# Kernel optimization log

Measured on AMD Instinct MI355X. Metric: run time of the kernel, lower is better.

The kernel has to match this reference:

```python
import jax, jax.numpy as jnp
import numpy as np

B, S, D, H, KH, DH, L, V, MULT = 1, 2048, 2048, 16, 2, 128, 4, 10000, 4
INNER = D * MULT
EPS = 1e-5


def layernorm(x, g, b):
    m = jnp.mean(x, axis=-1, keepdims=True)
    v = jnp.var(x, axis=-1, keepdims=True)
    return (x - m) * jax.lax.rsqrt(v + EPS) * g + b


def setup_inputs() -> dict:
    key = jax.random.key(0)
    ks = jax.random.split(key, 24)
    s = lambda *shape: 0.02
    inp = {
        'text': jax.random.randint(ks[0], (B, S), 0, V),
        'embed_w': jax.random.normal(ks[1], (V, D), jnp.float32) * 0.02,
        # model-level LayerNorm (applied after embed and after every block)
        'model_norm_g': jnp.ones((D,), jnp.float32),
        'model_norm_b': jnp.zeros((D,), jnp.float32),
        # per-block params, stacked on leading L axis
        'blk_norm_g': jnp.ones((L, D), jnp.float32),
        'blk_norm_b': jnp.zeros((L, D), jnp.float32),
        'attn_norm_g': jnp.ones((L, D), jnp.float32),  # RingAttention prenorm
        'attn_norm_b': jnp.zeros((L, D), jnp.float32),
        'wq': jax.random.normal(ks[2], (L, D, H * DH), jnp.float32) * 0.02,
        'wk': jax.random.normal(ks[3], (L, D, KH * DH), jnp.float32) * 0.02,
        'wv': jax.random.normal(ks[4], (L, D, KH * DH), jnp.float32) * 0.02,
        'wo': jax.random.normal(ks[5], (L, H * DH, D), jnp.float32) * 0.02,
        'qn_g': jnp.ones((L, DH), jnp.float32),  # qk_norm LayerNorm scales
        'kn_g': jnp.ones((L, DH), jnp.float32),
        'w1': jax.random.normal(ks[6], (L, D, INNER), jnp.float32) * 0.02,
        'b1': jnp.zeros((L, INNER), jnp.float32),
        'w2': jax.random.normal(ks[7], (L, INNER, D), jnp.float32) * 0.02,
        'b2': jnp.zeros((L, D), jnp.float32),
        # output head: LayerNorm + Linear(D, V)
        'head_norm_g': jnp.ones((D,), jnp.float32),
        'head_norm_b': jnp.zeros((D,), jnp.float32),
        'head_w': jax.random.normal(ks[8], (D, V), jnp.float32) * 0.02,
        'head_b': jnp.zeros((V,), jnp.float32),
    }
    return inp


def _attention(xn, wq, wk, wv, wo, qn_g, kn_g):
    # xn: [B,S,D] (already prenormed)
    q = (xn @ wq).reshape(B, S, H, DH)
    k = (xn @ wk).reshape(B, S, KH, DH)
    v = (xn @ wv).reshape(B, S, KH, DH)
    # qk-norm: LayerNorm over head dim with learnable scale
    q = layernorm(q, qn_g, 0.0)
    k = layernorm(k, kn_g, 0.0)
    # GQA: expand kv heads to query heads
    rep = H // KH
    k = jnp.repeat(k, rep, axis=2)  # [B,S,H,DH]
    v = jnp.repeat(v, rep, axis=2)
    scale = DH ** -0.5
    scores = jnp.einsum('bqhd,bkhd->bhqk', q, k) * scale  # [B,H,S,S]
    causal = jnp.tril(jnp.ones((S, S), bool))
    scores = jnp.where(causal, scores, jnp.finfo(scores.dtype).min)
    p = jax.nn.softmax(scores, axis=-1)
    out = jnp.einsum('bhqk,bkhd->bqhd', p, v).reshape(B, S, H * DH)
    return out @ wo


def reference(text, embed_w, model_norm_g, model_norm_b, blk_norm_g, blk_norm_b,
              attn_norm_g, attn_norm_b, wq, wk, wv, wo, qn_g, kn_g,
              w1, b1, w2, b2, head_norm_g, head_norm_b, head_w, head_b):
    x = embed_w[text]                                # [B,S,D]
    x = layernorm(x, model_norm_g, model_norm_b)
    for i in range(L):
        h = layernorm(x, blk_norm_g[i], blk_norm_b[i])       # block norm
        hn = layernorm(h, attn_norm_g[i], attn_norm_b[i])    # attn prenorm
        h = _attention(hn, wq[i], wk[i], wv[i], wo[i], qn_g[i], kn_g[i]) + h
        ff = jax.nn.gelu(h @ w1[i] + b1[i]) @ w2[i] + b2[i]
        x = ff + h
        x = layernorm(x, model_norm_g, model_norm_b)
    x = layernorm(x, head_norm_g, head_norm_b)
    return x @ head_w + head_b                       # [B,S,V] logits
```

## Files before the change

### kernel.cpp

```cpp
#include <hip/hip_runtime.h>
#include <math.h>

#define S_LEN 2048
#define DMODEL 2048
#define NHEAD 16
#define KVHEAD 2
#define DHEAD 128
#define NLAYER 4
#define VOCAB 10000
#define INNER_DIM 8192
#define LN_EPS 1e-5f
#define VOCAB_PAD 10240
#define QKVN 2560

typedef __attribute__((ext_vector_type(4))) float f32x4;
typedef __attribute__((ext_vector_type(2))) float f32x2;
typedef __attribute__((ext_vector_type(8))) short s16x8;
typedef __attribute__((ext_vector_type(4))) short s16x4;

__device__ __forceinline__ short f2bf(float f) {
  union { float f; unsigned u; } v; v.f = f;
  unsigned r = v.u + 0x7FFFu + ((v.u >> 16) & 1u);
  return (short)(r >> 16);
}

__device__ __forceinline__ float gelu_tanh(float x) {
  float z = 0.7978845608028654f * (x + 0.044715f * x * x * x);
  float t = __expf(-2.0f * fabsf(z));
  float th = (1.0f - t) / (1.0f + t);
  th = copysignf(th, z);
  return 0.5f * x * (1.0f + th);
}

__device__ __forceinline__ void glds16(const void* g, void* l) {
  __builtin_amdgcn_global_load_lds(
      (const __attribute__((address_space(1))) unsigned int*)g,
      (__attribute__((address_space(3))) unsigned int*)l, 16, 0, 0);
}

__global__ __launch_bounds__(256)
void wtrans_all(const float* __restrict__ wq, const float* __restrict__ wk,
                const float* __restrict__ wv, const float* __restrict__ wo,
                const float* __restrict__ w1, const float* __restrict__ w2,
                short* __restrict__ wqkvT, short* __restrict__ woT,
                short* __restrict__ w1T, short* __restrict__ w2T) {
  __shared__ float ld[64][65];
  int b = blockIdx.x;
  const float* W; short* WT; int gx, K;
  if (b < 1024)      { W = wq; WT = wqkvT; gx = 32; K = 2048; }
  else if (b < 1152) { b -= 1024; W = wk; WT = wqkvT + (size_t)2048 * 2048; gx = 4; K = 2048; }
  else if (b < 1280) { b -= 1152; W = wv; WT = wqkvT + (size_t)2304 * 2048; gx = 4; K = 2048; }
  else if (b < 2304) { b -= 1280; W = wo; WT = woT; gx = 32; K = 2048; }
  else if (b < 6400) { b -= 2304; W = w1; WT = w1T; gx = 128; K = 2048; }
  else               { b -= 6400; W = w2; WT = w2T; gx = 32; K = 8192; }
  const int N = gx * 64;
  const int n0 = (b % gx) * 64, k0 = (b / gx) * 64;
  const int tid = threadIdx.x;
  const int rbase = tid >> 4;
  const int c4 = (tid & 15) * 4;
#pragma unroll
  for (int q = 0; q < 4; ++q) {
    int kk = rbase + q * 16;
    f32x4 v = *(const f32x4*)(W + (size_t)(k0 + kk) * N + n0 + c4);
    ld[kk][c4 + 0] = v[0]; ld[kk][c4 + 1] = v[1];
    ld[kk][c4 + 2] = v[2]; ld[kk][c4 + 3] = v[3];
  }
  __syncthreads();
#pragma unroll
  for (int s = 0; s < 2; ++s) {
    int lin = tid + s * 256;
    int nn = lin >> 3;
    int ks = lin & 7;
    s16x8 o;
#pragma unroll
    for (int j = 0; j < 8; ++j) o[j] = f2bf(ld[ks * 8 + j][nn]);
    *(s16x8*)&WT[(size_t)(n0 + nn) * K + k0 + ks * 8] = o;
  }
}

__global__ __launch_bounds__(256)
void wtrans64(const float* __restrict__ W, short* __restrict__ WT,
              int K, int N, int NP) {
  __shared__ float ld[64][65];
  const int n0 = blockIdx.x * 64, k0 = blockIdx.y * 64;
  const int tid = threadIdx.x;
  const int rbase = tid >> 4;
  const int c4 = (tid & 15) * 4;
#pragma unroll
  for (int q = 0; q < 4; ++q) {
    int kk = rbase + q * 16;
    const float* wp = W + (size_t)(k0 + kk) * N + n0 + c4;
    float v0, v1, v2, v3;
    if (n0 + c4 + 3 < N) {
      f32x4 v = *(const f32x4*)wp;
      v0 = v[0]; v1 = v[1]; v2 = v[2]; v3 = v[3];
    } else {
      v0 = (n0 + c4 + 0 < N) ? wp[0] : 0.f;
      v1 = (n0 + c4 + 1 < N) ? wp[1] : 0.f;
      v2 = (n0 + c4 + 2 < N) ? wp[2] : 0.f;
      v3 = (n0 + c4 + 3 < N) ? wp[3] : 0.f;
    }
    ld[kk][c4 + 0] = v0; ld[kk][c4 + 1] = v1;
    ld[kk][c4 + 2] = v2; ld[kk][c4 + 3] = v3;
  }
  __syncthreads();
#pragma unroll
  for (int s = 0; s < 2; ++s) {
    int lin = tid + s * 256;
    int nn = lin >> 3;
    int ks = lin & 7;
    int n = n0 + nn;
    if (n < NP) {
      s16x8 o;
#pragma unroll
      for (int j = 0; j < 8; ++j)
        o[j] = (n < N) ? f2bf(ld[ks * 8 + j][nn]) : (short)0;
      *(s16x8*)&WT[(size_t)n * K + k0 + ks * 8] = o;
    }
  }
}

__device__ __forceinline__ void ln3_core(
    float (&v)[8], int tid, int wave,
    const float* __restrict__ mg, const float* __restrict__ mb,
    const float* __restrict__ bg, const float* __restrict__ bb,
    const float* __restrict__ ag, const float* __restrict__ ab,
    float* __restrict__ hbrow, short* __restrict__ hnrow,
    float rs[3][4], float rs2[3][4]) {
#pragma unroll
  for (int rnd = 0; rnd < 3; ++rnd) {
    float s = 0.f, s2 = 0.f;
#pragma unroll
    for (int i = 0; i < 8; ++i) { s += v[i]; s2 += v[i] * v[i]; }
#pragma unroll
    for (int off = 1; off < 64; off <<= 1) {
      s += __shfl_xor(s, off); s2 += __shfl_xor(s2, off);
    }
    if ((tid & 63) == 0) { rs[rnd][wave] = s; rs2[rnd][wave] = s2; }
    __syncthreads();
    s = rs[rnd][0] + rs[rnd][1] + rs[rnd][2] + rs[rnd][3];
    s2 = rs2[rnd][0] + rs2[rnd][1] + rs2[rnd][2] + rs2[rnd][3];
    const float mean = s * (1.f / DMODEL);
    const float var = s2 * (1.f / DMODEL) - mean * mean;
    const float rstd = rsqrtf(var + LN_EPS);
    const float* gg = (rnd == 0) ? mg : (rnd == 1) ? bg : ag;
    const float* bbv = (rnd == 0) ? mb : (rnd == 1) ? bb : ab;
#pragma unroll
    for (int i = 0; i < 8; ++i) {
      int idx = tid + i * 256;
      v[i] = (v[i] - mean) * rstd * gg[idx] + bbv[idx];
    }
    if (rnd == 1) {
#pragma unroll
      for (int i = 0; i < 8; ++i) hbrow[tid + i * 256] = v[i];
    }
  }
#pragma unroll
  for (int i = 0; i < 8; ++i) hnrow[tid + i * 256] = f2bf(v[i]);
}

__global__ __launch_bounds__(256)
void ln_triple(const float* __restrict__ in,
               const float* __restrict__ mg, const float* __restrict__ mb,
               const float* __restrict__ bg, const float* __restrict__ bb,
               const float* __restrict__ ag, const float* __restrict__ ab,
               float* __restrict__ hb, short* __restrict__ hn16) {
  const int row = blockIdx.x;
  const int tid = threadIdx.x;
  const int wave = tid >> 6;
  __shared__ float rs[3][4], rs2[3][4];
  float v[8];
  const float* x = in + (size_t)row * DMODEL;
#pragma unroll
  for (int i = 0; i < 8; ++i) v[i] = x[tid + i * 256];
  ln3_core(v, tid, wave, mg, mb, bg, bb, ag, ab,
           hb + (size_t)row * DMODEL, hn16 + (size_t)row * DMODEL, rs, rs2);
}

__global__ __launch_bounds__(256)
void embed_ln3(const int* __restrict__ text, const float* __restrict__ ew,
               const float* __restrict__ mg, const float* __restrict__ mb,
               const float* __restrict__ bg, const float* __restrict__ bb,
               const float* __restrict__ ag, const float* __restrict__ ab,
               float* __restrict__ hb, short* __restrict__ hn16) {
  const int row = blockIdx.x;
  const int tid = threadIdx.x;
  const int wave = tid >> 6;
  __shared__ float rs[3][4], rs2[3][4];
  float v[8];
  const float* x = ew + (size_t)text[row] * DMODEL;
#pragma unroll
  for (int i = 0; i < 8; ++i) v[i] = x[tid + i * 256];
  ln3_core(v, tid, wave, mg, mb, bg, bb, ag, ab,
           hb + (size_t)row * DMODEL, hn16 + (size_t)row * DMODEL, rs, rs2);
}

__global__ __launch_bounds__(256)
void ln_dual(const float* __restrict__ in,
             const float* __restrict__ mg, const float* __restrict__ mb,
             const float* __restrict__ hg, const float* __restrict__ hbv,
             short* __restrict__ out16) {
  const int row = blockIdx.x;
  const int tid = threadIdx.x;
  const int wave = tid >> 6;
  __shared__ float rs[2][4], rs2[2][4];
  float v[8];
  const float* x = in + (size_t)row * DMODEL;
#pragma unroll
  for (int i = 0; i < 8; ++i) v[i] = x[tid + i * 256];
#pragma unroll
  for (int rnd = 0; rnd < 2; ++rnd) {
    float s = 0.f, s2 = 0.f;
#pragma unroll
    for (int i = 0; i < 8; ++i) { s += v[i]; s2 += v[i] * v[i]; }
#pragma unroll
    for (int off = 1; off < 64; off <<= 1) {
      s += __shfl_xor(s, off); s2 += __shfl_xor(s2, off);
    }
    if ((tid & 63) == 0) { rs[rnd][wave] = s; rs2[rnd][wave] = s2; }
    __syncthreads();
    s = rs[rnd][0] + rs[rnd][1] + rs[rnd][2] + rs[rnd][3];
    s2 = rs2[rnd][0] + rs2[rnd][1] + rs2[rnd][2] + rs2[rnd][3];
    const float mean = s * (1.f / DMODEL);
    const float var = s2 * (1.f / DMODEL) - mean * mean;
    const float rstd = rsqrtf(var + LN_EPS);
    const float* gg = (rnd == 0) ? mg : hg;
    const float* bbv = (rnd == 0) ? mb : hbv;
#pragma unroll
    for (int i = 0; i < 8; ++i) {
      int idx = tid + i * 256;
      v[i] = (v[i] - mean) * rstd * gg[idx] + bbv[idx];
    }
  }
  short* o = out16 + (size_t)row * DMODEL;
#pragma unroll
  for (int i = 0; i < 8; ++i) o[tid + i * 256] = f2bf(v[i]);
}

__global__ __launch_bounds__(256)
void normqk_vtrans(const float* __restrict__ qkvf,
                   const float* __restrict__ qg, const float* __restrict__ kg,
                   short* __restrict__ qb16, short* __restrict__ kb16,
                   short* __restrict__ vt) {
  __shared__ float ld[64][65];
  if (blockIdx.x < 9216) {
    const int rowjob = blockIdx.x * 4 + (threadIdx.x >> 6);
    const int lane = threadIdx.x & 63;
    const int s = rowjob / 18, sub = rowjob - s * 18;
    const float* p; short* o; const float* g;
    if (sub < 16) {
      p = qkvf + (size_t)s * QKVN + sub * DHEAD;
      o = qb16 + ((size_t)s * 16 + sub) * DHEAD;
      g = qg;
    } else {
      p = qkvf + (size_t)s * QKVN + 2048 + (sub - 16) * DHEAD;
      o = kb16 + ((size_t)s * 2 + (sub - 16)) * DHEAD;
      g = kg;
    }
    f32x2 t = *(const f32x2*)(p + lane * 2);
    float sm = t[0] + t[1];
    float s2 = t[0] * t[0] + t[1] * t[1];
#pragma unroll
    for (int off = 1; off < 64; off <<= 1) {
      sm += __shfl_xor(sm, off); s2 += __shfl_xor(s2, off);
    }
    const float mean = sm * (1.f / DHEAD);
    const float var = s2 * (1.f / DHEAD) - mean * mean;
    const float rstd = rsqrtf(var + LN_EPS);
    o[lane * 2] = f2bf((t[0] - mean) * rstd * g[lane * 2]);
    o[lane * 2 + 1] = f2bf((t[1] - mean) * rstd * g[lane * 2 + 1]);
  } else {
    const int b = blockIdx.x - 9216;
    const int n0 = (b & 3) * 64, k0 = (b >> 2) * 64;
    const int tid = threadIdx.x;
    const int rbase = tid >> 4;
    const int c4 = (tid & 15) * 4;
#pragma unroll
    for (int q = 0; q < 4; ++q) {
      int kk = rbase + q * 16;
      f32x4 v = *(const f32x4*)(qkvf + (size_t)(k0 + kk) * QKVN + 2304 + n0 + c4);
      ld[kk][c4 + 0] = v[0]; ld[kk][c4 + 1] = v[1];
      ld[kk][c4 + 2] = v[2]; ld[kk][c4 + 3] = v[3];
    }
    __syncthreads();
#pragma unroll
    for (int s = 0; s < 2; ++s) {
      int lin = tid + s * 256;
      int nn = lin >> 3;
      int ks = lin & 7;
      s16x8 o;
#pragma unroll
      for (int j = 0; j < 8; ++j) o[j] = f2bf(ld[ks * 8 + j][nn]);
      *(s16x8*)&vt[(size_t)(n0 + nn) * S_LEN + k0 + ks * 8] = o;
    }
  }
}

template<int BM, int BN, int BK, int WM, int WN, int ACT, bool BIAS, bool RES,
         bool WF, bool WB>
__global__ __launch_bounds__(WM * WN * 64)
void gemm_db(const short* __restrict__ A, const short* __restrict__ BT,
             const float* __restrict__ bias, const float* __restrict__ res,
             float* __restrict__ Cf, short* __restrict__ Cb,
             int M, int N, int K) {
  constexpr int THREADS = WM * WN * 64;
  constexpr int MR = BM / WM / 16;
  constexpr int NR = BN / WN / 16;
  constexpr int KH = BK / 32;
  constexpr int SLOTS = BK / 8;
  constexpr int SMASK = SLOTS - 1;
  constexpr int RSH = (SLOTS == 8) ? 0 : 1;
  constexpr int CSH = (SLOTS == 8) ? 3 : 2;
  constexpr int NI = (BM * BK) / (THREADS * 8);
  __shared__ short As[2][BM * BK];
  __shared__ short Bs[2][BN * BK];
  const int tid = threadIdx.x;
  const int wave = tid >> 6, lane = tid & 63;
  const int g = lane >> 4, r = lane & 15;
  const int wm = wave / WN, wn = wave % WN;

  const int GY = gridDim.y;
  int lin = blockIdx.x + blockIdx.y * gridDim.x;
  int nwg = gridDim.x * GY;
  int sw = ((nwg & 7) == 0) ? ((lin & 7) * (nwg >> 3) + (lin >> 3)) : lin;
  const int bm = (sw % GY) * BM;
  const int bn = (sw / GY) * BN;

  const short* gsrc[2 * NI];
  short* ldst[2][2 * NI];
#pragma unroll
  for (int i = 0; i < NI; ++i) {
    int c = i * THREADS + tid;
    int row = c >> CSH;
    int slot = c & SMASK;
    int col = ((slot ^ ((row >> RSH) & SMASK)) << 3);
    gsrc[i] = A + (size_t)(bm + row) * K + col;
    gsrc[NI + i] = BT + (size_t)(bn + row) * K + col;
    int base = (i * THREADS + (wave << 6)) << 3;
    ldst[0][i] = &As[0][base]; ldst[0][NI + i] = &Bs[0][base];
    ldst[1][i] = &As[1][base]; ldst[1][NI + i] = &Bs[1][base];
  }

  f32x4 acc[MR][NR] = {};
  const int NT = K / BK;

#pragma unroll
  for (int i = 0; i < 2 * NI; ++i) glds16(gsrc[i], ldst[0][i]);
  asm volatile("s_waitcnt vmcnt(0)" ::: "memory");
  __syncthreads();

  for (int t = 0; t < NT; ++t) {
    const int cur = t & 1;
    const short* as = As[cur];
    const short* bs = Bs[cur];
    s16x8 bfr[NR][KH], af[MR / 2][KH];
#pragma unroll
    for (int n = 0; n < NR; ++n) {
      int rr = wn * (NR * 16) + n * 16 + r;
#pragma unroll
      for (int kk = 0; kk < KH; ++kk) {
        int lg = kk * 4 + g;
        bfr[n][kk] = *(const s16x8*)&bs[rr * BK + ((lg ^ ((rr >> RSH) & SMASK)) << 3)];
      }
    }
#pragma unroll
    for (int mm = 0; mm < MR / 2; ++mm) {
      int rr = wm * (MR * 16) + mm * 16 + r;
#pragma unroll
      for (int kk = 0; kk < KH; ++kk) {
        int lg = kk * 4 + g;
        af[mm][kk] = *(const s16x8*)&as[rr * BK + ((lg ^ ((rr >> RSH) & SMASK)) << 3)];
      }
    }
    if (t + 1 < NT) {
#pragma unroll
      for (int i = 0; i < 2 * NI; ++i) glds16(gsrc[i] + (t + 1) * BK, ldst[cur ^ 1][i]);
    }
    asm volatile("s_waitcnt lgkmcnt(0)" ::: "memory");
    __builtin_amdgcn_sched_barrier(0);
    __builtin_amdgcn_s_setprio(1);
#pragma unroll
    for (int mm = 0; mm < MR / 2; ++mm)
#pragma unroll
      for (int n = 0; n < NR; ++n)
#pragma unroll
        for (int kk = 0; kk < KH; ++kk)
          acc[mm][n] = __builtin_amdgcn_mfma_f32_16x16x32_bf16(af[mm][kk], bfr[n][kk], acc[mm][n], 0, 0, 0);
    __builtin_amdgcn_s_setprio(0);
    __builtin_amdgcn_s_barrier();
#pragma unroll
    for (int mm = 0; mm < MR / 2; ++mm) {
      int rr = wm * (MR * 16) + (MR / 2 + mm) * 16 + r;
#pragma unroll
      for (int kk = 0; kk < KH; ++kk) {
        int lg = kk * 4 + g;
        af[mm][kk] = *(const s16x8*)&as[rr * BK + ((lg ^ ((rr >> RSH) & SMASK)) << 3)];
      }
    }
    asm volatile("s_waitcnt lgkmcnt(0)" ::: "memory");
    __builtin_amdgcn_sched_barrier(0);
    __builtin_amdgcn_s_setprio(1);
#pragma unroll
    for (int mm = 0; mm < MR / 2; ++mm)
#pragma unroll
      for (int n = 0; n < NR; ++n)
#pragma unroll
        for (int kk = 0; kk < KH; ++kk)
          acc[MR / 2 + mm][n] = __builtin_amdgcn_mfma_f32_16x16x32_bf16(af[mm][kk], bfr[n][kk], acc[MR / 2 + mm][n], 0, 0, 0);
    __builtin_amdgcn_s_setprio(0);
    __syncthreads();
  }

#pragma unroll
  for (int m = 0; m < MR; ++m) {
    int row = bm + wm * (MR * 16) + m * 16 + g * 4;
#pragma unroll
    for (int n = 0; n < NR; ++n) {
      int col = bn + wn * (NR * 16) + n * 16 + r;
      if (col < N) {
#pragma unroll
        for (int j = 0; j < 4; ++j) {
          float v = acc[m][n][j];
          if (BIAS) v += bias[col];
          if (ACT) v = gelu_tanh(v);
          if (RES) v += res[(size_t)(row + j) * N + col];
          if (WF) Cf[(size_t)(row + j) * N + col] = v;
          if (WB) Cb[(size_t)(row + j) * N + col] = f2bf(v);
        }
      }
    }
  }
}

template<int ACT, bool BIAS, bool WF, bool WB>
__global__ __launch_bounds__(512, 2)
void gemm_8ph(const short* __restrict__ A, const short* __restrict__ BT,
              const float* __restrict__ bias,
              float* __restrict__ Cf, short* __restrict__ Cb,
              int M, int N, int K) {
  __shared__ short As[2][2][128 * 64];
  __shared__ short Bs[2][2][128 * 64];
  const int tid = threadIdx.x;
  const int wave = tid >> 6, lane = tid & 63;
  const int g = lane >> 4, r = lane & 15;
  const int wm = wave >> 2, wn = wave & 3;

  const int GY = gridDim.y;
  int lin = blockIdx.x + blockIdx.y * gridDim.x;
  int nwg = gridDim.x * GY;
  int sw = (lin & 7) * (nwg >> 3) + (lin >> 3);
  const int bm = (sw % GY) * 256;
  const int bn = (sw / GY) * 256;

  int rl[2], csw[2], ldo[2];
#pragma unroll
  for (int i = 0; i < 2; ++i) {
    int c = i * 512 + tid;
    rl[i] = c >> 3;
    csw[i] = (((c & 7) ^ (rl[i] & 7)) << 3);
    ldo[i] = (i * 512 + (wave << 6)) << 3;
  }
  const int NT = K >> 6;

  auto stA = [&](int t, int h, int d) {
#pragma unroll
    for (int i = 0; i < 2; ++i)
      glds16(A + (size_t)(bm + h * 128 + rl[i]) * K + t * 64 + csw[i], &As[d][h][ldo[i]]);
  };
  auto stB = [&](int t, int h, int d) {
#pragma unroll
    for (int i = 0; i < 2; ++i)
      glds16(BT + (size_t)(bn + h * 128 + rl[i]) * K + t * 64 + csw[i], &Bs[d][h][ldo[i]]);
  };

  stA(0, 0, 0); stA(0, 1, 0); stB(0, 0, 0); stB(0, 1, 0);
  stA(1, 0, 1);
  asm volatile("s_waitcnt vmcnt(2)" ::: "memory");
  asm volatile("s_barrier" ::: "memory");

  f32x4 acc[8][4] = {};
  s16x8 af[4][2], bf0[2][2], bf1[2][2];
  const int brow = (wn & 1) * 64;
  const int U = NT >> 1;

  for (int u = 0; u < U; ++u) {
    const int t1 = 2 * u + 1;
    const int q0 = (2 * u + 2 < NT) ? 2 * u + 2 : 0;
    const int q1 = (2 * u + 3 < NT) ? 2 * u + 3 : 0;
#pragma unroll
    for (int d = 0; d < 2; ++d) {
      const short* as = As[d][wm];
      const short* bsl = Bs[d][wn >> 1];
#pragma unroll
      for (int m = 0; m < 4; ++m)
#pragma unroll
        for (int kk = 0; kk < 2; ++kk)
          af[m][kk] = *(const s16x8*)&as[(m * 16 + r) * 64 + (((kk * 4 + g) ^ (r & 7)) << 3)];
#pragma unroll
      for (int n = 0; n < 2; ++n)
#pragma unroll
        for (int kk = 0; kk < 2; ++kk)
          bf0[n][kk] = *(const s16x8*)&bsl[(brow + n * 16 + r) * 64 + (((kk * 4 + g) ^ (r & 7)) << 3)];
      if (d == 0) stA(t1, 1, 1); else stA(q0, 1, 0);
      asm volatile("s_waitcnt lgkmcnt(0)" ::: "memory");
      __builtin_amdgcn_sched_barrier(0);
      __builtin_amdgcn_s_setprio(1);
#pragma unroll
      for (int m = 0; m < 4; ++m)
#pragma unroll
        for (int n = 0; n < 2; ++n)
#pragma unroll
          for (int kk = 0; kk < 2; ++kk)
            acc[m][n] = __builtin_amdgcn_mfma_f32_16x16x32_bf16(af[m][kk], bf0[n][kk], acc[m][n], 0, 0, 0);
      __builtin_amdgcn_s_setprio(0);
      asm volatile("s_barrier" ::: "memory");
#pragma unroll
      for (int n = 0; n < 2; ++n)
#pragma unroll
        for (int kk = 0; kk < 2; ++kk)
          bf1[n][kk] = *(const s16x8*)&bsl[(brow + (n + 2) * 16 + r) * 64 + (((kk * 4 + g) ^ (r & 7)) << 3)];
      if (d == 0) stB(t1, 0, 1); else stB(q0, 0, 0);
      asm volatile("s_waitcnt lgkmcnt(0)" ::: "memory");
      __builtin_amdgcn_sched_barrier(0);
      __builtin_amdgcn_s_setprio(1);
#pragma unroll
      for (int m = 0; m < 4; ++m)
#pragma unroll
        for (int n = 0; n < 2; ++n)
#pragma unroll
          for (int kk = 0; kk < 2; ++kk)
            acc[m][n + 2] = __builtin_amdgcn_mfma_f32_16x16x32_bf16(af[m][kk], bf1[n][kk], acc[m][n + 2], 0, 0, 0);
      __builtin_amdgcn_s_setprio(0);
      asm volatile("s_barrier" ::: "memory");
#pragma unroll
      for (int m = 0; m < 4; ++m)
#pragma unroll
        for (int kk = 0; kk < 2; ++kk)
          af[m][kk] = *(const s16x8*)&as[((m + 4) * 16 + r) * 64 + (((kk * 4 + g) ^ (r & 7)) << 3)];
      if (d == 0) stB(t1, 1, 1); else stB(q0, 1, 0);
      asm volatile("s_waitcnt lgkmcnt(0)" ::: "memory");
      __builtin_amdgcn_sched_barrier(0);
      __builtin_amdgcn_s_setprio(1);
#pragma unroll
      for (int m = 0; m < 4; ++m)
#pragma unroll
        for (int n = 0; n < 2; ++n)
#pragma unroll
          for (int kk = 0; kk < 2; ++kk)
            acc[m + 4][n + 2] = __builtin_amdgcn_mfma_f32_16x16x32_bf16(af[m][kk], bf1[n][kk], acc[m + 4][n + 2], 0, 0, 0);
      __builtin_amdgcn_s_setprio(0);
      asm volatile("s_barrier" ::: "memory");
      if (d == 0) stA(q0, 0, 0); else stA(q1, 0, 1);
      __builtin_amdgcn_s_setprio(1);
#pragma unroll
      for (int m = 0; m < 4; ++m)
#pragma unroll
        for (int n = 0; n < 2; ++n)
#pragma unroll
          for (int kk = 0; kk < 2; ++kk)
            acc[m + 4][n] = __builtin_amdgcn_mfma_f32_16x16x32_bf16(af[m][kk], bf0[n][kk], acc[m + 4][n], 0, 0, 0);
      __builtin_amdgcn_s_setprio(0);
      asm volatile("s_waitcnt vmcnt(2)" ::: "memory");
      asm volatile("s_barrier" ::: "memory");
    }
  }
  asm volatile("s_waitcnt vmcnt(0)" ::: "memory");

#pragma unroll
  for (int m = 0; m < 8; ++m) {
    int row = bm + wm * 128 + m * 16 + g * 4;
#pragma unroll
    for (int n = 0; n < 4; ++n) {
      int col = bn + wn * 64 + n * 16 + r;
      if (col < N) {
#pragma unroll
        for (int j = 0; j < 4; ++j) {
          float v = acc[m][n][j];
          if (BIAS) v += bias[col];
          if (ACT) v = gelu_tanh(v);
          if (WF) Cf[(size_t)(row + j) * N + col] = v;
          if (WB) Cb[(size_t)(row + j) * N + col] = f2bf(v);
        }
      }
    }
  }
}

__global__ __launch_bounds__(256)
void attn_fwd2(const short* __restrict__ qbuf, const short* __restrict__ kbuf,
               const short* __restrict__ vtb, short* __restrict__ obuf) {
  __shared__ short Qs[64 * 128];
  __shared__ short Ks[64 * 128];
  __shared__ short Vt[128 * 64];
  __shared__ short Ps[4][16][88];
  const int tid = threadIdx.x;
  int lin = blockIdx.x + blockIdx.y * gridDim.x;
  int sw = (lin & 7) * 32 + (lin >> 3);
  const int pair = sw & 15;
  const int h = sw >> 4;
  const int kh = h >> 3;
  const int wave = tid >> 6, lane = tid & 63;
  const int g = lane >> 4, r = lane & 15;
  const float scale = 0.08838834764831845f;

#pragma unroll
  for (int half = 0; half < 2; ++half) {
    const int qt = half ? (31 - pair) : pair;
    const int qbase = qt * 64;
    __builtin_amdgcn_s_barrier();
#pragma unroll
    for (int i = 0; i < 4; ++i) {
      int c = i * 256 + tid;
      int row = c >> 4;
      int scol = (((c & 15) ^ (row & 7)) << 3);
      glds16(qbuf + (size_t)(qbase + row) * DMODEL + h * DHEAD + scol,
             &Qs[(i * 256 + (wave << 6)) << 3]);
    }
    f32x4 O[8] = {};
    float mst[4], lst[4];
#pragma unroll
    for (int j = 0; j < 4; ++j) { mst[j] = -1e30f; lst[j] = 0.f; }
    s16x8 aq[4];

    for (int jt = 0; jt <= qt; ++jt) {
      const int jb = jt * 64;
      if (jt) __builtin_amdgcn_s_barrier();
#pragma unroll
      for (int i = 0; i < 4; ++i) {
        int c = i * 256 + tid;
        int row = c >> 4;
        int scol = (((c & 15) ^ (row & 7)) << 3);
        glds16(kbuf + (size_t)(jb + row) * 256 + kh * DHEAD + scol,
               &Ks[(i * 256 + (wave << 6)) << 3]);
      }
#pragma unroll
      for (int i = 0; i < 4; ++i) {
        int c = i * 256 + tid;
        int row = c >> 3;
        int scol = (((c & 7) ^ (row & 7)) << 3);
        glds16(vtb + (size_t)(kh * 128 + row) * S_LEN + jb + scol,
               &Vt[(i * 256 + (wave << 6)) << 3]);
      }
      asm volatile("s_waitcnt vmcnt(0)" ::: "memory");
      __builtin_amdgcn_s_barrier();
      if (jt == 0) {
#pragma unroll
        for (int kc = 0; kc < 4; ++kc) {
          int rr = wave * 16 + r;
          aq[kc] = *(const s16x8*)&Qs[rr * 128 + ((((kc << 2) | g) ^ (rr & 7)) << 3)];
        }
      }
      f32x4 sc[4] = {};
      __builtin_amdgcn_s_setprio(1);
#pragma unroll
      for (int n = 0; n < 4; ++n) {
        int rr = n * 16 + r;
#pragma unroll
        for (int kc = 0; kc < 4; ++kc) {
          s16x8 bk = *(const s16x8*)&Ks[rr * 128 + ((((kc << 2) | g) ^ (rr & 7)) << 3)];
          sc[n] = __builtin_amdgcn_mfma_f32_16x16x32_bf16(aq[kc], bk, sc[n], 0, 0, 0);
        }
      }
      __builtin_amdgcn_s_setprio(0);
      if (jt == qt) {
#pragma unroll
        for (int j = 0; j < 4; ++j) {
          int irow = qbase + wave * 16 + g * 4 + j;
#pragma unroll
          for (int n = 0; n < 4; ++n) {
            int jcol = jb + n * 16 + r;
            sc[n][j] = (jcol <= irow) ? sc[n][j] * scale : -1e30f;
          }
        }
      } else {
#pragma unroll
        for (int j = 0; j < 4; ++j)
#pragma unroll
          for (int n = 0; n < 4; ++n) sc[n][j] *= scale;
      }
      float pmax[4], alpha[4], rsum[4];
#pragma unroll
      for (int j = 0; j < 4; ++j)
        pmax[j] = fmaxf(fmaxf(sc[0][j], sc[1][j]), fmaxf(sc[2][j], sc[3][j]));
#pragma unroll
      for (int off = 1; off < 16; off <<= 1)
#pragma unroll
        for (int j = 0; j < 4; ++j) pmax[j] = fmaxf(pmax[j], __shfl_xor(pmax[j], off));
#pragma unroll
      for (int j = 0; j < 4; ++j) {
        float mnew = fmaxf(mst[j], pmax[j]);
        alpha[j] = __expf(mst[j] - mnew);
        mst[j] = mnew;
#pragma unroll
        for (int n = 0; n < 4; ++n) sc[n][j] = __expf(sc[n][j] - mnew);
        rsum[j] = (sc[0][j] + sc[1][j]) + (sc[2][j] + sc[3][j]);
      }
#pragma unroll
      for (int off = 1; off < 16; off <<= 1)
#pragma unroll
        for (int j = 0; j < 4; ++j) rsum[j] += __shfl_xor(rsum[j], off);
#pragma unroll
      for (int j = 0; j < 4; ++j) lst[j] = lst[j] * alpha[j] + rsum[j];
#pragma unroll
      for (int d = 0; d < 8; ++d)
#pragma unroll
        for (int j = 0; j < 4; ++j) O[d][j] *= alpha[j];
#pragma unroll
      for (int j = 0; j < 4; ++j)
#pragma unroll
        for (int n = 0; n < 4; ++n)
          Ps[wave][g * 4 + j][n * 16 + r] = f2bf(sc[n][j]);
      s16x8 pa0 = *(const s16x8*)&Ps[wave][r][g * 8];
      s16x8 pa1 = *(const s16x8*)&Ps[wave][r][32 + g * 8];
      __builtin_amdgcn_s_setprio(1);
#pragma unroll
      for (int d = 0; d < 8; ++d) {
        int dd = d * 16 + r;
        s16x8 b0 = *(const s16x8*)&Vt[dd * 64 + ((g ^ (dd & 7)) << 3)];
        s16x8 b1 = *(const s16x8*)&Vt[dd * 64 + (((4 + g) ^ (dd & 7)) << 3)];
        O[d] = __builtin_amdgcn_mfma_f32_16x16x32_bf16(pa0, b0, O[d], 0, 0, 0);
        O[d] = __builtin_amdgcn_mfma_f32_16x16x32_bf16(pa1, b1, O[d], 0, 0, 0);
      }
      __builtin_amdgcn_s_setprio(0);
    }
    float linv[4];
#pragma unroll
    for (int j = 0; j < 4; ++j) linv[j] = 1.f / lst[j];
#pragma unroll
    for (int d = 0; d < 8; ++d)
#pragma unroll
      for (int j = 0; j < 4; ++j)
        obuf[(size_t)(qbase + wave * 16 + g * 4 + j) * DMODEL + h * DHEAD + d * 16 + r] =
            f2bf(O[d][j] * linv[j]);
  }
}

extern "C" void kernel_launch(void* const* d_in, const int* in_sizes, int n_in,
                              void* d_out, int out_size, void* d_ws, size_t ws_size,
                              hipStream_t stream) {
  const int* text = (const int*)d_in[0];
  const float* embed_w = (const float*)d_in[1];
  const float* model_g = (const float*)d_in[2];
  const float* model_b = (const float*)d_in[3];
  const float* blk_g = (const float*)d_in[4];
  const float* blk_b = (const float*)d_in[5];
  const float* attn_g = (const float*)d_in[6];
  const float* attn_b = (const float*)d_in[7];
  const float* wq = (const float*)d_in[8];
  const float* wk = (const float*)d_in[9];
  const float* wv = (const float*)d_in[10];
  const float* wo = (const float*)d_in[11];
  const float* qn_g = (const float*)d_in[12];
  const float* kn_g = (const float*)d_in[13];
  const float* w1 = (const float*)d_in[14];
  const float* b1 = (const float*)d_in[15];
  const float* w2 = (const float*)d_in[16];
  const float* b2 = (const float*)d_in[17];
  const float* head_g = (const float*)d_in[18];
  const float* head_b = (const float*)d_in[19];
  const float* head_w = (const float*)d_in[20];
  const float* head_bias = (const float*)d_in[21];
  float* out = (float*)d_out;

  const size_t SD = (size_t)S_LEN * DMODEL;
  const size_t SKV = (size_t)S_LEN * KVHEAD * DHEAD;
  const size_t SI = (size_t)S_LEN * INNER_DIM;
  const size_t WD = (size_t)DMODEL * DMODEL;
  const size_t WKV = (size_t)DMODEL * KVHEAD * DHEAD;
  const size_t WI = (size_t)DMODEL * INNER_DIM;

  char* p = (char*)d_ws;
  float* xres  = (float*)p; p += SD * 4;
  float* hb    = (float*)p; p += SD * 4;
  float* h2    = (float*)p; p += SD * 4;
  float* qkvf  = (float*)p; p += (size_t)S_LEN * QKVN * 4;
  short* hn16  = (short*)p; p += SD * 2;
  short* h216  = (short*)p; p += SD * 2;
  short* ao16  = (short*)p; p += SD * 2;
  short* ffi16 = (short*)p; p += SI * 2;
  short* qb16  = (short*)p; p += SD * 2;
  short* kb16  = (short*)p; p += SKV * 2;
  short* vt16  = (short*)p; p += SKV * 2;
  short* wqkvT = (short*)p; p += (size_t)QKVN * DMODEL * 2;
  short* woT   = (short*)p; p += WD * 2;
  short* w1T   = (short*)p; p += WI * 2;
  short* w2T   = (short*)p; p += WI * 2;
  short* headT = w1T;

  dim3 blk(256);
  embed_ln3<<<S_LEN, blk, 0, stream>>>(text, embed_w, model_g, model_b,
                                       blk_g, blk_b, attn_g, attn_b, hb, hn16);

  for (int i = 0; i < NLAYER; ++i) {
    wtrans_all<<<10496, blk, 0, stream>>>(
        wq + (size_t)i * WD, wk + (size_t)i * WKV, wv + (size_t)i * WKV,
        wo + (size_t)i * WD, w1 + (size_t)i * WI, w2 + (size_t)i * WI,
        wqkvT, woT, w1T, w2T);

    gemm_db<128, 128, 64, 2, 2, 0, false, false, true, false>
        <<<dim3(QKVN / 128, S_LEN / 128), blk, 0, stream>>>(
        hn16, wqkvT, nullptr, nullptr, qkvf, nullptr, S_LEN, QKVN, DMODEL);

    normqk_vtrans<<<9344, blk, 0, stream>>>(
        qkvf, qn_g + i * DHEAD, kn_g + i * DHEAD, qb16, kb16, vt16);

    attn_fwd2<<<dim3(16, 16), blk, 0, stream>>>(qb16, kb16, vt16, ao16);

    gemm_db<128, 128, 64, 2, 2, 0, false, true, true, true>
        <<<dim3(DMODEL / 128, S_LEN / 128), blk, 0, stream>>>(
        ao16, woT, nullptr, hb, h2, h216, S_LEN, DMODEL, DMODEL);
    gemm_8ph<1, true, false, true>
        <<<dim3(INNER_DIM / 256, S_LEN / 256), dim3(512), 0, stream>>>(
        h216, w1T, b1 + (size_t)i * INNER_DIM, nullptr, ffi16, S_LEN, INNER_DIM, DMODEL);
    gemm_db<128, 128, 64, 2, 2, 0, true, true, true, false>
        <<<dim3(DMODEL / 128, S_LEN / 128), blk, 0, stream>>>(
        ffi16, w2T, b2 + (size_t)i * DMODEL, h2, xres, nullptr, S_LEN, DMODEL, INNER_DIM);

    if (i + 1 < NLAYER) {
      ln_triple<<<S_LEN, blk, 0, stream>>>(
          xres, model_g, model_b,
          blk_g + (i + 1) * DMODEL, blk_b + (i + 1) * DMODEL,
          attn_g + (i + 1) * DMODEL, attn_b + (i + 1) * DMODEL, hb, hn16);
    }
  }

  wtrans64<<<dim3(VOCAB_PAD / 64, 32), blk, 0, stream>>>(head_w, headT, DMODEL, VOCAB, VOCAB_PAD);
  ln_dual<<<S_LEN, blk, 0, stream>>>(xres, model_g, model_b, head_g, head_b, hn16);
  gemm_8ph<0, true, true, false>
      <<<dim3(VOCAB_PAD / 256, S_LEN / 256), dim3(512), 0, stream>>>(
      hn16, headT, head_bias, out, nullptr, S_LEN, VOCAB, DMODEL);
}
```

Measured before the change: 1.709 ms.

## Fuse QK layernorm into QKV GEMM epilogue and overlap V loads in attention

```diff
diff --git a/kernel.cpp b/kernel.cpp
--- a/kernel.cpp
+++ b/kernel.cpp
@@ -238,61 +238,28 @@
 }
 
 __global__ __launch_bounds__(256)
-void normqk_vtrans(const float* __restrict__ qkvf,
-                   const float* __restrict__ qg, const float* __restrict__ kg,
-                   short* __restrict__ qb16, short* __restrict__ kb16,
-                   short* __restrict__ vt) {
-  __shared__ float ld[64][65];
-  if (blockIdx.x < 9216) {
-    const int rowjob = blockIdx.x * 4 + (threadIdx.x >> 6);
-    const int lane = threadIdx.x & 63;
-    const int s = rowjob / 18, sub = rowjob - s * 18;
-    const float* p; short* o; const float* g;
-    if (sub < 16) {
-      p = qkvf + (size_t)s * QKVN + sub * DHEAD;
-      o = qb16 + ((size_t)s * 16 + sub) * DHEAD;
-      g = qg;
-    } else {
-      p = qkvf + (size_t)s * QKVN + 2048 + (sub - 16) * DHEAD;
-      o = kb16 + ((size_t)s * 2 + (sub - 16)) * DHEAD;
-      g = kg;
-    }
-    f32x2 t = *(const f32x2*)(p + lane * 2);
-    float sm = t[0] + t[1];
-    float s2 = t[0] * t[0] + t[1] * t[1];
-#pragma unroll
-    for (int off = 1; off < 64; off <<= 1) {
-      sm += __shfl_xor(sm, off); s2 += __shfl_xor(s2, off);
-    }
-    const float mean = sm * (1.f / DHEAD);
-    const float var = s2 * (1.f / DHEAD) - mean * mean;
-    const float rstd = rsqrtf(var + LN_EPS);
-    o[lane * 2] = f2bf((t[0] - mean) * rstd * g[lane * 2]);
-    o[lane * 2 + 1] = f2bf((t[1] - mean) * rstd * g[lane * 2 + 1]);
-  } else {
-    const int b = blockIdx.x - 9216;
-    const int n0 = (b & 3) * 64, k0 = (b >> 2) * 64;
-    const int tid = threadIdx.x;
-    const int rbase = tid >> 4;
-    const int c4 = (tid & 15) * 4;
-#pragma unroll
-    for (int q = 0; q < 4; ++q) {
-      int kk = rbase + q * 16;
-      f32x4 v = *(const f32x4*)(qkvf + (size_t)(k0 + kk) * QKVN + 2304 + n0 + c4);
-      ld[kk][c4 + 0] = v[0]; ld[kk][c4 + 1] = v[1];
-      ld[kk][c4 + 2] = v[2]; ld[kk][c4 + 3] = v[3];
-    }
-    __syncthreads();
-#pragma unroll
-    for (int s = 0; s < 2; ++s) {
-      int lin = tid + s * 256;
-      int nn = lin >> 3;
-      int ks = lin & 7;
-      s16x8 o;
-#pragma unroll
-      for (int j = 0; j < 8; ++j) o[j] = f2bf(ld[ks * 8 + j][nn]);
-      *(s16x8*)&vt[(size_t)(n0 + nn) * S_LEN + k0 + ks * 8] = o;
-    }
+void vtrans_b16(const short* __restrict__ vb, short* __restrict__ vt) {
+  __shared__ short ld[64][72];
+  const int b = blockIdx.x;
+  const int n0 = (b & 3) * 64, k0 = (b >> 2) * 64;
+  const int tid = threadIdx.x;
+  {
+    int row = tid >> 2, s0 = (tid & 3) * 16;
+    s16x8 a = *(const s16x8*)(vb + (size_t)(k0 + row) * 256 + n0 + s0);
+    s16x8 c = *(const s16x8*)(vb + (size_t)(k0 + row) * 256 + n0 + s0 + 8);
+    *(s16x8*)&ld[row][s0] = a;
+    *(s16x8*)&ld[row][s0 + 8] = c;
+  }
+  __syncthreads();
+  {
+    int d = tid >> 2, seg = tid & 3;
+    s16x8 o0, o1;
+#pragma unroll
+    for (int i = 0; i < 8; ++i) o0[i] = ld[seg * 16 + i][d];
+#pragma unroll
+    for (int i = 0; i < 8; ++i) o1[i] = ld[seg * 16 + 8 + i][d];
+    *(s16x8*)&vt[(size_t)(n0 + d) * S_LEN + k0 + seg * 16] = o0;
+    *(s16x8*)&vt[(size_t)(n0 + d) * S_LEN + k0 + seg * 16 + 8] = o1;
   }
 }
 
@@ -432,6 +399,171 @@
   }
 }
 
+__global__ __launch_bounds__(256)
+void gemm_qkv(const short* __restrict__ A, const short* __restrict__ BT,
+              const float* __restrict__ qg, const float* __restrict__ kg,
+              short* __restrict__ qb, short* __restrict__ kb,
+              short* __restrict__ vb, int M, int K) {
+  __shared__ short As[2][128 * 64];
+  __shared__ short Bs[2][128 * 64];
+  __shared__ float rsm[2][128], rs2m[2][128];
+  const int tid = threadIdx.x;
+  const int wave = tid >> 6, lane = tid & 63;
+  const int g = lane >> 4, r = lane & 15;
+  const int wm = wave >> 1, wn = wave & 1;
+
+  const int GY = gridDim.y;
+  int lin = blockIdx.x + blockIdx.y * gridDim.x;
+  int nwg = gridDim.x * GY;
+  int sw = (lin & 7) * (nwg >> 3) + (lin >> 3);
+  const int bm = (sw % GY) * 128;
+  const int bn = (sw / GY) * 128;
+
+  const short* gsrc[8];
+  short* ldst[2][8];
+#pragma unroll
+  for (int i = 0; i < 4; ++i) {
+    int c = i * 256 + tid;
+    int row = c >> 3;
+    int slot = c & 7;
+    int col = ((slot ^ (row & 7)) << 3);
+    gsrc[i] = A + (size_t)(bm + row) * K + col;
+    gsrc[4 + i] = BT + (size_t)(bn + row) * K + col;
+    int base = (i * 256 + (wave << 6)) << 3;
+    ldst[0][i] = &As[0][base]; ldst[0][4 + i] = &Bs[0][base];
+    ldst[1][i] = &As[1][base]; ldst[1][4 + i] = &Bs[1][base];
+  }
+
+  f32x4 acc[4][4] = {};
+  const int NT = K >> 6;
+
+#pragma unroll
+  for (int i = 0; i < 8; ++i) glds16(gsrc[i], ldst[0][i]);
+  asm volatile("s_waitcnt vmcnt(0)" ::: "memory");
+  __syncthreads();
+
+  for (int t = 0; t < NT; ++t) {
+    const int cur = t & 1;
+    const short* as = As[cur];
+    const short* bs = Bs[cur];
+    s16x8 bfr[4][2], af[2][2];
+#pragma unroll
+    for (int n = 0; n < 4; ++n) {
+      int rr = wn * 64 + n * 16 + r;
+#pragma unroll
+      for (int kk = 0; kk < 2; ++kk) {
+        int lg = kk * 4 + g;
+        bfr[n][kk] = *(const s16x8*)&bs[rr * 64 + ((lg ^ (rr & 7)) << 3)];
+      }
+    }
+#pragma unroll
+    for (int mm = 0; mm < 2; ++mm) {
+      int rr = wm * 64 + mm * 16 + r;
+#pragma unroll
+      for (int kk = 0; kk < 2; ++kk) {
+        int lg = kk * 4 + g;
+        af[mm][kk] = *(const s16x8*)&as[rr * 64 + ((lg ^ (rr & 7)) << 3)];
+      }
+    }
+    if (t + 1 < NT) {
+#pragma unroll
+      for (int i = 0; i < 8; ++i) glds16(gsrc[i] + (t + 1) * 64, ldst[cur ^ 1][i]);
+    }
+    asm volatile("s_waitcnt lgkmcnt(0)" ::: "memory");
+    __builtin_amdgcn_sched_barrier(0);
+    __builtin_amdgcn_s_setprio(1);
+#pragma unroll
+    for (int mm = 0; mm < 2; ++mm)
+#pragma unroll
+      for (int n = 0; n < 4; ++n)
+#pragma unroll
+        for (int kk = 0; kk < 2; ++kk)
+          acc[mm][n] = __builtin_amdgcn_mfma_f32_16x16x32_bf16(af[mm][kk], bfr[n][kk], acc[mm][n], 0, 0, 0);
+    __builtin_amdgcn_s_setprio(0);
+    __builtin_amdgcn_s_barrier();
+#pragma unroll
+    for (int mm = 0; mm < 2; ++mm) {
+      int rr = wm * 64 + (2 + mm) * 16 + r;
+#pragma unroll
+      for (int kk = 0; kk < 2; ++kk) {
+        int lg = kk * 4 + g;
+        af[mm][kk] = *(const s16x8*)&as[rr * 64 + ((lg ^ (rr & 7)) << 3)];
+      }
+    }
+    asm volatile("s_waitcnt lgkmcnt(0)" ::: "memory");
+    __builtin_amdgcn_sched_barrier(0);
+    __builtin_amdgcn_s_setprio(1);
+#pragma unroll
+    for (int mm = 0; mm < 2; ++mm)
+#pragma unroll
+      for (int n = 0; n < 4; ++n)
+#pragma unroll
+        for (int kk = 0; kk < 2; ++kk)
+          acc[2 + mm][n] = __builtin_amdgcn_mfma_f32_16x16x32_bf16(af[mm][kk], bfr[n][kk], acc[2 + mm][n], 0, 0, 0);
+    __builtin_amdgcn_s_setprio(0);
+    __syncthreads();
+  }
+
+  if (bn >= 2304) {
+#pragma unroll
+    for (int m = 0; m < 4; ++m) {
+      int row = bm + wm * 64 + m * 16 + g * 4;
+#pragma unroll
+      for (int n = 0; n < 4; ++n) {
+        int cl = wn * 64 + n * 16 + r;
+#pragma unroll
+        for (int j = 0; j < 4; ++j)
+          vb[(size_t)(row + j) * 256 + (bn - 2304) + cl] = f2bf(acc[m][n][j]);
+      }
+    }
+  } else {
+    float ms[4][4], m2[4][4];
+#pragma unroll
+    for (int m = 0; m < 4; ++m)
+#pragma unroll
+      for (int j = 0; j < 4; ++j) {
+        float s = 0.f, s2 = 0.f;
+#pragma unroll
+        for (int n = 0; n < 4; ++n) { float v = acc[m][n][j]; s += v; s2 += v * v; }
+#pragma unroll
+        for (int off = 1; off < 16; off <<= 1) {
+          s += __shfl_xor(s, off); s2 += __shfl_xor(s2, off);
+        }
+        ms[m][j] = s; m2[m][j] = s2;
+      }
+    if (r == 0) {
+#pragma unroll
+      for (int m = 0; m < 4; ++m)
+#pragma unroll
+        for (int j = 0; j < 4; ++j) {
+          int rl = wm * 64 + m * 16 + g * 4 + j;
+          rsm[wn][rl] = ms[m][j]; rs2m[wn][rl] = m2[m][j];
+        }
+    }
+    __syncthreads();
+    const float* gv = (bn < 2048) ? qg : kg;
+#pragma unroll
+    for (int m = 0; m < 4; ++m)
+#pragma unroll
+      for (int j = 0; j < 4; ++j) {
+        int rl = wm * 64 + m * 16 + g * 4 + j;
+        float s = rsm[0][rl] + rsm[1][rl];
+        float s2 = rs2m[0][rl] + rs2m[1][rl];
+        float mean = s * (1.f / 128.f);
+        float var = s2 * (1.f / 128.f) - mean * mean;
+        float rstd = rsqrtf(var + LN_EPS);
+        int srow = bm + rl;
+#pragma unroll
+        for (int n = 0; n < 4; ++n) {
+          int cl = wn * 64 + n * 16 + r;
+          float v = (acc[m][n][j] - mean) * rstd * gv[cl];
+          if (bn < 2048) qb[(size_t)srow * 2048 + bn + cl] = f2bf(v);
+          else kb[(size_t)srow * 256 + (bn - 2048) + cl] = f2bf(v);
+        }
+      }
+  }
+}
+
 template<int ACT, bool BIAS, bool WF, bool WB>
 __global__ __launch_bounds__(512, 2)
 void gemm_8ph(const short* __restrict__ A, const short* __restrict__ BT,
@@ -587,7 +719,7 @@
 }
 
 __global__ __launch_bounds__(256)
-void attn_fwd2(const short* __restrict__ qbuf, const short* __restrict__ kbuf,
+void attn_fwd3(const short* __restrict__ qbuf, const short* __restrict__ kbuf,
                const short* __restrict__ vtb, short* __restrict__ obuf) {
   __shared__ short Qs[64 * 128];
   __shared__ short Ks[64 * 128];
@@ -641,7 +773,7 @@
         glds16(vtb + (size_t)(kh * 128 + row) * S_LEN + jb + scol,
                &Vt[(i * 256 + (wave << 6)) << 3]);
       }
-      asm volatile("s_waitcnt vmcnt(0)" ::: "memory");
+      asm volatile("s_waitcnt vmcnt(4)" ::: "memory");
       __builtin_amdgcn_s_barrier();
       if (jt == 0) {
 #pragma unroll
@@ -705,6 +837,8 @@
       for (int d = 0; d < 8; ++d)
 #pragma unroll
         for (int j = 0; j < 4; ++j) O[d][j] *= alpha[j];
+      asm volatile("s_waitcnt vmcnt(0)" ::: "memory");
+      __builtin_amdgcn_s_barrier();
 #pragma unroll
       for (int j = 0; j < 4; ++j)
 #pragma unroll
@@ -773,13 +907,13 @@
   float* xres  = (float*)p; p += SD * 4;
   float* hb    = (float*)p; p += SD * 4;
   float* h2    = (float*)p; p += SD * 4;
-  float* qkvf  = (float*)p; p += (size_t)S_LEN * QKVN * 4;
   short* hn16  = (short*)p; p += SD * 2;
   short* h216  = (short*)p; p += SD * 2;
   short* ao16  = (short*)p; p += SD * 2;
   short* ffi16 = (short*)p; p += SI * 2;
   short* qb16  = (short*)p; p += SD * 2;
   short* kb16  = (short*)p; p += SKV * 2;
+  short* vb16  = (short*)p; p += SKV * 2;
   short* vt16  = (short*)p; p += SKV * 2;
   short* wqkvT = (short*)p; p += (size_t)QKVN * DMODEL * 2;
   short* woT   = (short*)p; p += WD * 2;
@@ -797,14 +931,13 @@
         wo + (size_t)i * WD, w1 + (size_t)i * WI, w2 + (size_t)i * WI,
         wqkvT, woT, w1T, w2T);
 
-    gemm_db<128, 128, 64, 2, 2, 0, false, false, true, false>
-        <<<dim3(QKVN / 128, S_LEN / 128), blk, 0, stream>>>(
-        hn16, wqkvT, nullptr, nullptr, qkvf, nullptr, S_LEN, QKVN, DMODEL);
-
-    normqk_vtrans<<<9344, blk, 0, stream>>>(
-        qkvf, qn_g + i * DHEAD, kn_g + i * DHEAD, qb16, kb16, vt16);
-
-    attn_fwd2<<<dim3(16, 16), blk, 0, stream>>>(qb16, kb16, vt16, ao16);
+    gemm_qkv<<<dim3(QKVN / 128, S_LEN / 128), blk, 0, stream>>>(
+        hn16, wqkvT, qn_g + i * DHEAD, kn_g + i * DHEAD,
+        qb16, kb16, vb16, S_LEN, DMODEL);
+
+    vtrans_b16<<<128, blk, 0, stream>>>(vb16, vt16);
+
+    attn_fwd3<<<dim3(16, 16), blk, 0, stream>>>(qb16, kb16, vt16, ao16);
 
     gemm_db<128, 128, 64, 2, 2, 0, false, true, true, true>
         <<<dim3(DMODEL / 128, S_LEN / 128), blk, 0, stream>>>(
```

New measurement: 1.658 ms. -3.0%, faster.
